# Kernel optimization log

Hardware: AMD Instinct MI355X
Metric: run time of the kernel (lower is better)

The kernel has to match this reference:

```python
import jax, jax.numpy as jnp
import numpy as np

CLS_NUM, INPUT_DIM, BATCH = 1024, 512, 16384
TAU = 0.1       # gumbel-softmax temperature from F.gumbel_softmax(sim, tau=0.1)
EPS = 1e-12     # F.normalize eps


def _l2norm(x):
    # F.normalize(x, p=2, dim=1)
    n = jnp.sqrt(jnp.sum(x * x, axis=1, keepdims=True))
    return x / jnp.maximum(n, EPS)


def setup_inputs() -> dict:
    key = jax.random.key(0)
    k1, k2, k3 = jax.random.split(key, 3)
    # xavier_uniform bound for [cls_num, input_dim]
    bound = float(np.sqrt(6.0 / (CLS_NUM + INPUT_DIM)))
    return {
        "input": jax.random.normal(k1, (BATCH, INPUT_DIM), dtype=jnp.float32),
        "prototypes_para": jax.random.uniform(k2, (CLS_NUM, INPUT_DIM), dtype=jnp.float32, minval=-bound, maxval=bound),
        "gumbel_u": jax.random.uniform(k3, (BATCH, CLS_NUM), dtype=jnp.float32, minval=1e-6, maxval=1.0 - 1e-6),
    }


def reference(input, prototypes_para, gumbel_u):
    x = _l2norm(input)                 # [B, D]
    p = _l2norm(prototypes_para)       # [K, D]
    # Original: broadcast x and p to [B, K, D] (via multiply-by-ones) then cosine.
    # Since both are unit-norm, cosine similarity == dot product -> one matmul.
    # Input is .detach()'d in the original, so stop_gradient on x here.
    sim = jax.lax.stop_gradient(x) @ p.T                    # [B, K]
    # Gumbel-softmax (soft): softmax((logits + gumbel)/tau)
    g = -jnp.log(-jnp.log(gumbel_u))
    e = jax.nn.softmax((sim + g) / TAU, axis=-1)            # [B, K]
    pt = jnp.einsum('bk,kv->bv', e, p)                      # [B, D]
    sim_loss = jnp.mean(1.0 - jnp.einsum('bk,bk->b', e, sim))
    # Nested i!=j pairwise cosine loop == sum of P P^T minus its diagonal
    ppt = p @ p.T                                           # [K, K]
    div_loss = jnp.sum(ppt) - jnp.sum(jnp.diagonal(ppt))
    return pt, p, sim_loss, div_loss
```

## Files before the change

### kernel.cpp

```cpp
#include <hip/hip_runtime.h>
#include <hip/hip_bf16.h>
#include <math.h>

#define B  16384
#define K  1024
#define D  512
#define TAU_INV 10.0f
#define EPS 1e-12f

typedef unsigned short ushort_t;

#define OUT_PT   0
#define OUT_P    (B*D)
#define OUT_SIM  (B*D + K*D)
#define OUT_DIV  (B*D + K*D + 1)

#define WS_DIAG  2
#define WS_RED   1024
#define WS_COL   2048
#define WS_SIM   32768
#define WS_PH    (WS_SIM + B*K)
#define WS_PTH   (WS_PH + (K*D)/2)


typedef _Float16 half8 __attribute__((ext_vector_type(8)));
typedef float f32x4 __attribute__((ext_vector_type(4)));

__device__ __forceinline__ float wave_reduce_sum(float v) {
    #pragma unroll
    for (int off = 32; off >= 1; off >>= 1) v += __shfl_down(v, off);
    return v;
}
__device__ __forceinline__ float wave_reduce_max(float v) {
    #pragma unroll
    for (int off = 32; off >= 1; off >>= 1) v = fmaxf(v, __shfl_down(v, off));
    return v;
}

__device__ __forceinline__ ushort_t f2h(float f) {
    _Float16 h = (_Float16)f;
    return __builtin_bit_cast(ushort_t, h);
}

__device__ __forceinline__ void async16(const void* g, void* l) {
    __builtin_amdgcn_global_load_lds(
        (const __attribute__((address_space(1))) unsigned int*)g,
        (__attribute__((address_space(3))) unsigned int*)l, 16, 0, 0);
}

__global__ __launch_bounds__(256) void zero_ws(float* ws) {
    int t = threadIdx.x;
    if (t < 16) ws[t] = 0.0f;
    ws[WS_COL + t] = 0.0f;
    ws[WS_COL + 256 + t] = 0.0f;
}

__global__ __launch_bounds__(256) void norm_p_kernel(const float* __restrict__ proto,
                                                     float* __restrict__ out,
                                                     float* __restrict__ ws) {
    int wid = threadIdx.x >> 6, lane = threadIdx.x & 63;
    int row = blockIdx.x * 4 + wid;
    const float4* pr = (const float4*)(proto + (size_t)row * D);
    float4 a = pr[lane * 2], b = pr[lane * 2 + 1];
    float ss = a.x*a.x + a.y*a.y + a.z*a.z + a.w*a.w
             + b.x*b.x + b.y*b.y + b.z*b.z + b.w*b.w;
    ss = wave_reduce_sum(ss);
    ss = __shfl(ss, 0);
    float inv = 1.0f / fmaxf(sqrtf(ss), EPS);
    float4* po = (float4*)(out + OUT_P + (size_t)row * D);
    po[lane * 2]     = make_float4(a.x*inv, a.y*inv, a.z*inv, a.w*inv);
    po[lane * 2 + 1] = make_float4(b.x*inv, b.y*inv, b.z*inv, b.w*inv);
    __shared__ float red[4];
    if (lane == 0) red[wid] = ss * inv * inv;
    __syncthreads();
    if (threadIdx.x == 0)
        atomicAdd(ws + WS_DIAG, red[0] + red[1] + red[2] + red[3]);
}

__global__ __launch_bounds__(256) void pcvt_kernel(const float* __restrict__ out,
                                                   ushort_t* __restrict__ Ph) {
    int k = blockIdx.x, tid = threadIdx.x;
    const float2* pr = (const float2*)(out + OUT_P + (size_t)k * D);
    float2 v = pr[tid];
    *(ushort2*)(Ph + (size_t)k * D + 2 * tid) = make_ushort2(f2h(v.x), f2h(v.y));
}

__global__ __launch_bounds__(256) void ptcvt_kernel(const float* __restrict__ out,
                                                    ushort_t* __restrict__ PT) {
    __shared__ float tile[64][65];
    int k0 = blockIdx.x * 64, d0 = blockIdx.y * 64;
    int tid = threadIdx.x;
    const float* phat = out + OUT_P;
    #pragma unroll
    for (int i = tid; i < 64 * 64; i += 256) {
        int kk = i >> 6, dd = i & 63;
        tile[dd][kk] = phat[(size_t)(k0 + kk) * D + d0 + dd];
    }
    __syncthreads();
    #pragma unroll
    for (int i = tid; i < 64 * 64; i += 256) {
        int dd = i >> 6, kk = i & 63;
        PT[(size_t)(d0 + dd) * K + k0 + kk] = f2h(tile[dd][kk]);
    }
}

__global__ __launch_bounds__(256) void col_partial(const float* __restrict__ out,
                                                   float* __restrict__ ws) {
    int d = threadIdx.x * 2;
    const float* p = out + OUT_P + (size_t)blockIdx.x * 32 * D;
    float sx = 0.0f, sy = 0.0f;
    #pragma unroll
    for (int kk = 0; kk < 32; ++kk) {
        float2 v = *(const float2*)(p + (size_t)kk * D + d);
        sx += v.x; sy += v.y;
    }
    atomicAdd(ws + WS_COL + d, sx);
    atomicAdd(ws + WS_COL + d + 1, sy);
}

__global__ __launch_bounds__(256) void xcvt_kernel(const float* __restrict__ x,
                                                   ushort_t* __restrict__ Xh) {
    int wid = threadIdx.x >> 6, lane = threadIdx.x & 63;
    int row = blockIdx.x * 4 + wid;
    const float4* xr = (const float4*)(x + (size_t)row * D);
    float4 a = xr[lane * 2], b = xr[lane * 2 + 1];
    float ss = a.x*a.x + a.y*a.y + a.z*a.z + a.w*a.w
             + b.x*b.x + b.y*b.y + b.z*b.z + b.w*b.w;
    ss = wave_reduce_sum(ss);
    ss = __shfl(ss, 0);
    float inv = 1.0f / fmaxf(sqrtf(ss), EPS);
    ushort4 h0 = make_ushort4(f2h(a.x*inv), f2h(a.y*inv), f2h(a.z*inv), f2h(a.w*inv));
    ushort4 h1 = make_ushort4(f2h(b.x*inv), f2h(b.y*inv), f2h(b.z*inv), f2h(b.w*inv));
    ushort4* xo = (ushort4*)(Xh + (size_t)row * D);
    xo[lane * 2]     = h0;
    xo[lane * 2 + 1] = h1;
}

template<int LDA, int LDB, int LDC, int SEGK>
__global__ __launch_bounds__(256) void gemm_bt(const ushort_t* __restrict__ A,
                                               const ushort_t* __restrict__ Bm,
                                               float* __restrict__ C) {
    __shared__ __align__(16) ushort_t As[128 * 32];
    __shared__ __align__(16) ushort_t Bs[128 * 32];
    int tid = threadIdx.x;
    int wid = tid >> 6, lane = tid & 63;
    int quad = lane >> 4, l16 = lane & 15;
    int wm = (wid & 1) * 64, wn = (wid >> 1) * 64;
    int bn0 = blockIdx.x * 128, bm0 = blockIdx.y * 128;
    int ldrow = lane >> 2;
    int lcol  = (lane & 3) * 8;

    f32x4 acc[4][4] = {};

    ushort_t* AsW0 = As + (wid * 16) * 32;
    ushort_t* AsW1 = As + (64 + wid * 16) * 32;
    ushort_t* BsW0 = Bs + (wid * 16) * 32;
    ushort_t* BsW1 = Bs + (64 + wid * 16) * 32;

    const ushort_t* Ab = A + (size_t)(bm0 + wid * 16 + ldrow) * LDA + lcol;
    const ushort_t* Bb = Bm + (size_t)(bn0 + wid * 16 + ldrow) * LDB + lcol;

    for (int kc = 0; kc < SEGK; kc += 32) {
        async16(Ab + kc, AsW0);
        async16(Ab + kc + (size_t)64 * LDA, AsW1);
        async16(Bb + kc, BsW0);
        async16(Bb + kc + (size_t)64 * LDB, BsW1);
        __syncthreads();
        half8 af[4], bg[4];
        #pragma unroll
        for (int i = 0; i < 4; ++i)
            af[i] = *(const half8*)(As + (wm + 16 * i + l16) * 32 + quad * 8);
        #pragma unroll
        for (int j = 0; j < 4; ++j)
            bg[j] = *(const half8*)(Bs + (wn + 16 * j + l16) * 32 + quad * 8);
        #pragma unroll
        for (int i = 0; i < 4; ++i)
            #pragma unroll
            for (int j = 0; j < 4; ++j)
                acc[i][j] = __builtin_amdgcn_mfma_f32_16x16x32_f16(af[i], bg[j], acc[i][j], 0, 0, 0);
        __syncthreads();
    }
    #pragma unroll
    for (int i = 0; i < 4; ++i) {
        #pragma unroll
        for (int j = 0; j < 4; ++j) {
            #pragma unroll
            for (int r = 0; r < 4; ++r) {
                int row = bm0 + wm + 16 * i + quad * 4 + r;
                int col = bn0 + wn + 16 * j + l16;
                C[(size_t)row * LDC + col] = acc[i][j][r];
            }
        }
    }
}

__global__ __launch_bounds__(256) void softmax_rows(const float* __restrict__ u,
                                                    float* __restrict__ ws) {
    float* simbuf = ws + WS_SIM;
    int tid = threadIdx.x;
    int wid = tid >> 6, lane = tid & 63;
    int gw = blockIdx.x * 4 + wid;
    float dotacc = 0.0f;

    for (int r = 0; r < 4; ++r) {
        int row = gw + 4096 * r;
        const float4* srow = (const float4*)(simbuf + (size_t)row * K);
        const float4* urow = (const float4*)(u + (size_t)row * K);
        float4 s[4], z[4];
        #pragma unroll
        for (int j = 0; j < 4; ++j) {
            float4 sv = srow[lane + 64 * j];
            float4 uu = urow[lane + 64 * j];
            s[j] = sv;
            z[j].x = (sv.x - logf(-logf(uu.x))) * TAU_INV;
            z[j].y = (sv.y - logf(-logf(uu.y))) * TAU_INV;
            z[j].z = (sv.z - logf(-logf(uu.z))) * TAU_INV;
            z[j].w = (sv.w - logf(-logf(uu.w))) * TAU_INV;
        }
        float m = z[0].x;
        #pragma unroll
        for (int j = 0; j < 4; ++j)
            m = fmaxf(m, fmaxf(fmaxf(z[j].x, z[j].y), fmaxf(z[j].z, z[j].w)));
        m = wave_reduce_max(m);
        m = __shfl(m, 0);

        float4 e[4];
        float l = 0.0f;
        #pragma unroll
        for (int j = 0; j < 4; ++j) {
            e[j].x = expf(z[j].x - m);
            e[j].y = expf(z[j].y - m);
            e[j].z = expf(z[j].z - m);
            e[j].w = expf(z[j].w - m);
            l += e[j].x + e[j].y + e[j].z + e[j].w;
        }
        l = wave_reduce_sum(l);
        l = __shfl(l, 0);
        float inv = 1.0f / l;

        ushort_t* erow = (ushort_t*)(simbuf + (size_t)row * K);
        #pragma unroll
        for (int j = 0; j < 4; ++j) {
            float ex = e[j].x * inv, ey = e[j].y * inv,
                  ez = e[j].z * inv, ew = e[j].w * inv;
            *(ushort4*)(erow + 4 * (lane + 64 * j)) =
                make_ushort4(f2h(ex), f2h(ey), f2h(ez), f2h(ew));
            dotacc += ex * s[j].x + ey * s[j].y + ez * s[j].z + ew * s[j].w;
        }
    }

    dotacc = wave_reduce_sum(dotacc);
    __shared__ float red[4];
    if (lane == 0) red[wid] = dotacc;
    __syncthreads();
    if (tid == 0) ws[WS_RED + blockIdx.x] = red[0] + red[1] + red[2] + red[3];
}

__global__ __launch_bounds__(256) void finalize_kernel(float* __restrict__ out,
                                                       const float* __restrict__ ws) {
    int tid = threadIdx.x, wid = tid >> 6, lane = tid & 63;
    float vdot = 0.0f;
    #pragma unroll
    for (int i = 0; i < 4; ++i) vdot += ws[WS_RED + tid + 256 * i];
    float c0 = ws[WS_COL + tid], c1 = ws[WS_COL + 256 + tid];
    float vssq = c0 * c0 + c1 * c1;
    vdot = wave_reduce_sum(vdot);
    vssq = wave_reduce_sum(vssq);
    __shared__ float rd[4], rs[4];
    if (lane == 0) { rd[wid] = vdot; rs[wid] = vssq; }
    __syncthreads();
    if (tid == 0) {
        float dot = rd[0] + rd[1] + rd[2] + rd[3];
        float ssq = rs[0] + rs[1] + rs[2] + rs[3];
        out[OUT_SIM] = 1.0f - dot * (1.0f / (float)B);
        out[OUT_DIV] = ssq - ws[WS_DIAG];
    }
}

extern "C" void kernel_launch(void* const* d_in, const int* in_sizes, int n_in,
                              void* d_out, int out_size, void* d_ws, size_t ws_size,
                              hipStream_t stream) {
    const float* input  = (const float*)d_in[0];
    const float* proto  = (const float*)d_in[1];
    const float* gumbel = (const float*)d_in[2];
    float* out = (float*)d_out;
    float* ws  = (float*)d_ws;

    ushort_t* Xh  = (ushort_t*)(out + OUT_PT);
    ushort_t* Ph  = (ushort_t*)(ws + WS_PH);
    ushort_t* PTh = (ushort_t*)(ws + WS_PTH);
    ushort_t* Eh  = (ushort_t*)(ws + WS_SIM);
    float* sim = ws + WS_SIM;

    zero_ws<<<1, 256, 0, stream>>>(ws);
    norm_p_kernel<<<K / 4, 256, 0, stream>>>(proto, out, ws);
    pcvt_kernel<<<K, 256, 0, stream>>>(out, Ph);
    {
        dim3 grid(K / 64, D / 64);
        ptcvt_kernel<<<grid, 256, 0, stream>>>(out, PTh);
    }
    col_partial<<<K / 32, 256, 0, stream>>>(out, ws);
    xcvt_kernel<<<B / 4, 256, 0, stream>>>(input, Xh);
    {
        dim3 grid(K / 128, B / 128);
        gemm_bt<512, 512, K, 512><<<grid, 256, 0, stream>>>(Xh, Ph, sim);
    }
    softmax_rows<<<1024, 256, 0, stream>>>(gumbel, ws);
    {
        dim3 grid(D / 128, B / 128);
        gemm_bt<2048, 1024, D, 1024><<<grid, 256, 0, stream>>>(Eh, PTh, out + OUT_PT);
    }
    finalize_kernel<<<1, 256, 0, stream>>>(out, ws);
}
```

Measured before the change: 234.1 us.

## Store sim matrix as fp16 and use LDS-free direct-load MFMA GEMM

The similarity matrix is now written as fp16 instead of fp32, which halves the B×K intermediate traffic between the first GEMM and the softmax. Softmax reads and writes that fp16 buffer in place. Both GEMMs swap LDS staging with syncthreads for direct global loads into registers, using a 32x128 per-wave tile and launch_bounds occupancy 2. This drops barriers and LDS traffic but depends on cache hits for reuse. Storing sim in fp16 lowers the precision of sim_loss.

```diff
diff --git a/kernel.cpp b/kernel.cpp
--- a/kernel.cpp
+++ b/kernel.cpp
@@ -19,7 +19,7 @@
 #define WS_RED   1024
 #define WS_COL   2048
 #define WS_SIM   32768
-#define WS_PH    (WS_SIM + B*K)
+#define WS_PH    (WS_SIM + (B*K)/2)
 #define WS_PTH   (WS_PH + (K*D)/2)
 
 
@@ -41,11 +41,8 @@
     _Float16 h = (_Float16)f;
     return __builtin_bit_cast(ushort_t, h);
 }
-
-__device__ __forceinline__ void async16(const void* g, void* l) {
-    __builtin_amdgcn_global_load_lds(
-        (const __attribute__((address_space(1))) unsigned int*)g,
-        (__attribute__((address_space(3))) unsigned int*)l, 16, 0, 0);
+__device__ __forceinline__ float h2f(ushort_t u) {
+    return (float)__builtin_bit_cast(_Float16, u);
 }
 
 __global__ __launch_bounds__(256) void zero_ws(float* ws) {
@@ -136,59 +133,49 @@
     xo[lane * 2 + 1] = h1;
 }
 
-template<int LDA, int LDB, int LDC, int SEGK>
-__global__ __launch_bounds__(256) void gemm_bt(const ushort_t* __restrict__ A,
-                                               const ushort_t* __restrict__ Bm,
-                                               float* __restrict__ C) {
-    __shared__ __align__(16) ushort_t As[128 * 32];
-    __shared__ __align__(16) ushort_t Bs[128 * 32];
+template<int LDA, int LDB, int LDC, int KK, bool F16C>
+__global__ __launch_bounds__(256, 2) void gemm_direct(const ushort_t* __restrict__ A,
+                                                      const ushort_t* __restrict__ Bm,
+                                                      void* __restrict__ Cv) {
     int tid = threadIdx.x;
     int wid = tid >> 6, lane = tid & 63;
     int quad = lane >> 4, l16 = lane & 15;
-    int wm = (wid & 1) * 64, wn = (wid >> 1) * 64;
-    int bn0 = blockIdx.x * 128, bm0 = blockIdx.y * 128;
-    int ldrow = lane >> 2;
-    int lcol  = (lane & 3) * 8;
-
-    f32x4 acc[4][4] = {};
-
-    ushort_t* AsW0 = As + (wid * 16) * 32;
-    ushort_t* AsW1 = As + (64 + wid * 16) * 32;
-    ushort_t* BsW0 = Bs + (wid * 16) * 32;
-    ushort_t* BsW1 = Bs + (64 + wid * 16) * 32;
-
-    const ushort_t* Ab = A + (size_t)(bm0 + wid * 16 + ldrow) * LDA + lcol;
-    const ushort_t* Bb = Bm + (size_t)(bn0 + wid * 16 + ldrow) * LDB + lcol;
-
-    for (int kc = 0; kc < SEGK; kc += 32) {
-        async16(Ab + kc, AsW0);
-        async16(Ab + kc + (size_t)64 * LDA, AsW1);
-        async16(Bb + kc, BsW0);
-        async16(Bb + kc + (size_t)64 * LDB, BsW1);
-        __syncthreads();
-        half8 af[4], bg[4];
-        #pragma unroll
-        for (int i = 0; i < 4; ++i)
-            af[i] = *(const half8*)(As + (wm + 16 * i + l16) * 32 + quad * 8);
-        #pragma unroll
-        for (int j = 0; j < 4; ++j)
-            bg[j] = *(const half8*)(Bs + (wn + 16 * j + l16) * 32 + quad * 8);
-        #pragma unroll
-        for (int i = 0; i < 4; ++i)
+    int m0 = blockIdx.y * 128 + wid * 32;
+    int n0 = blockIdx.x * 128;
+
+    const ushort_t* Ap = A + (size_t)(m0 + l16) * LDA + quad * 8;
+    const ushort_t* Bp = Bm + (size_t)(n0 + l16) * LDB + quad * 8;
+
+    f32x4 acc[2][8] = {};
+
+    #pragma unroll 8
+    for (int kc = 0; kc < KK; kc += 32) {
+        half8 af[2], bg[8];
+        #pragma unroll
+        for (int i = 0; i < 2; ++i)
+            af[i] = *(const half8*)(Ap + kc + (size_t)(16 * i) * LDA);
+        #pragma unroll
+        for (int j = 0; j < 8; ++j)
+            bg[j] = *(const half8*)(Bp + kc + (size_t)(16 * j) * LDB);
+        #pragma unroll
+        for (int i = 0; i < 2; ++i)
             #pragma unroll
-            for (int j = 0; j < 4; ++j)
+            for (int j = 0; j < 8; ++j)
                 acc[i][j] = __builtin_amdgcn_mfma_f32_16x16x32_f16(af[i], bg[j], acc[i][j], 0, 0, 0);
-        __syncthreads();
-    }
-    #pragma unroll
-    for (int i = 0; i < 4; ++i) {
-        #pragma unroll
-        for (int j = 0; j < 4; ++j) {
+    }
+
+    #pragma unroll
+    for (int i = 0; i < 2; ++i) {
+        #pragma unroll
+        for (int j = 0; j < 8; ++j) {
             #pragma unroll
             for (int r = 0; r < 4; ++r) {
-                int row = bm0 + wm + 16 * i + quad * 4 + r;
-                int col = bn0 + wn + 16 * j + l16;
-                C[(size_t)row * LDC + col] = acc[i][j][r];
+                int row = m0 + 16 * i + quad * 4 + r;
+                int col = n0 + 16 * j + l16;
+                if (F16C)
+                    ((ushort_t*)Cv)[(size_t)row * LDC + col] = f2h(acc[i][j][r]);
+                else
+                    ((float*)Cv)[(size_t)row * LDC + col] = acc[i][j][r];
             }
         }
     }
@@ -196,7 +183,7 @@
 
 __global__ __launch_bounds__(256) void softmax_rows(const float* __restrict__ u,
                                                     float* __restrict__ ws) {
-    float* simbuf = ws + WS_SIM;
+    ushort_t* simh = (ushort_t*)(ws + WS_SIM);
     int tid = threadIdx.x;
     int wid = tid >> 6, lane = tid & 63;
     int gw = blockIdx.x * 4 + wid;
@@ -204,18 +191,18 @@
 
     for (int r = 0; r < 4; ++r) {
         int row = gw + 4096 * r;
-        const float4* srow = (const float4*)(simbuf + (size_t)row * K);
+        ushort4* srow = (ushort4*)(simh + (size_t)row * K);
         const float4* urow = (const float4*)(u + (size_t)row * K);
         float4 s[4], z[4];
         #pragma unroll
         for (int j = 0; j < 4; ++j) {
-            float4 sv = srow[lane + 64 * j];
+            ushort4 sh = srow[lane + 64 * j];
             float4 uu = urow[lane + 64 * j];
-            s[j] = sv;
-            z[j].x = (sv.x - logf(-logf(uu.x))) * TAU_INV;
-            z[j].y = (sv.y - logf(-logf(uu.y))) * TAU_INV;
-            z[j].z = (sv.z - logf(-logf(uu.z))) * TAU_INV;
-            z[j].w = (sv.w - logf(-logf(uu.w))) * TAU_INV;
+            s[j] = make_float4(h2f(sh.x), h2f(sh.y), h2f(sh.z), h2f(sh.w));
+            z[j].x = (s[j].x - logf(-logf(uu.x))) * TAU_INV;
+            z[j].y = (s[j].y - logf(-logf(uu.y))) * TAU_INV;
+            z[j].z = (s[j].z - logf(-logf(uu.z))) * TAU_INV;
+            z[j].w = (s[j].w - logf(-logf(uu.w))) * TAU_INV;
         }
         float m = z[0].x;
         #pragma unroll
@@ -238,13 +225,11 @@
         l = __shfl(l, 0);
         float inv = 1.0f / l;
 
-        ushort_t* erow = (ushort_t*)(simbuf + (size_t)row * K);
         #pragma unroll
         for (int j = 0; j < 4; ++j) {
             float ex = e[j].x * inv, ey = e[j].y * inv,
                   ez = e[j].z * inv, ew = e[j].w * inv;
-            *(ushort4*)(erow + 4 * (lane + 64 * j)) =
-                make_ushort4(f2h(ex), f2h(ey), f2h(ez), f2h(ew));
+            srow[lane + 64 * j] = make_ushort4(f2h(ex), f2h(ey), f2h(ez), f2h(ew));
             dotacc += ex * s[j].x + ey * s[j].y + ez * s[j].z + ew * s[j].w;
         }
     }
@@ -286,11 +271,10 @@
     float* out = (float*)d_out;
     float* ws  = (float*)d_ws;
 
-    ushort_t* Xh  = (ushort_t*)(out + OUT_PT);
-    ushort_t* Ph  = (ushort_t*)(ws + WS_PH);
-    ushort_t* PTh = (ushort_t*)(ws + WS_PTH);
-    ushort_t* Eh  = (ushort_t*)(ws + WS_SIM);
-    float* sim = ws + WS_SIM;
+    ushort_t* Xh   = (ushort_t*)(out + OUT_PT);
+    ushort_t* Ph   = (ushort_t*)(ws + WS_PH);
+    ushort_t* PTh  = (ushort_t*)(ws + WS_PTH);
+    ushort_t* simh = (ushort_t*)(ws + WS_SIM);
 
     zero_ws<<<1, 256, 0, stream>>>(ws);
     norm_p_kernel<<<K / 4, 256, 0, stream>>>(proto, out, ws);
@@ -303,12 +287,12 @@
     xcvt_kernel<<<B / 4, 256, 0, stream>>>(input, Xh);
     {
         dim3 grid(K / 128, B / 128);
-        gemm_bt<512, 512, K, 512><<<grid, 256, 0, stream>>>(Xh, Ph, sim);
+        gemm_direct<512, 512, K, 512, true><<<grid, 256, 0, stream>>>(Xh, Ph, simh);
     }
     softmax_rows<<<1024, 256, 0, stream>>>(gumbel, ws);
     {
         dim3 grid(D / 128, B / 128);
-        gemm_bt<2048, 1024, D, 1024><<<grid, 256, 0, stream>>>(Eh, PTh, out + OUT_PT);
+        gemm_direct<1024, 1024, D, 1024, false><<<grid, 256, 0, stream>>>(simh, PTh, out + OUT_PT);
     }
     finalize_kernel<<<1, 256, 0, stream>>>(out, ws);
 }
```

Result: slower. 317.3 us (+35.5%).
